# Optimization experiments

Measured on AMD Instinct MI355X. Metric: run time of the kernel, lower is better.

## Reference

```python
import jax, jax.numpy as jnp
import numpy as np

EPS = 1e-8  # args.epsilon
B, N, D = 2, 512, 64


def _cmul(ar, ai, br, bi):
    # complex Hadamard: (ar+i ai)(br+i bi)
    return ar * br - ai * bi, ar * bi + ai * br


def _clin(Z, W, b):
    # complex linear: Z [B,2,N,din], W [2,dout,din], b [2,dout]
    yr = Z[:, 0] @ W[0].T - Z[:, 1] @ W[1].T + b[0]
    yi = Z[:, 0] @ W[1].T + Z[:, 1] @ W[0].T + b[1]
    return yr, yi


def setup_inputs() -> dict:
    key = jax.random.key(0)
    ks = jax.random.split(key, 12)
    s = 1.0 / np.sqrt(D)
    inp = {
        "Z_q": jax.random.normal(ks[0], (B, 2, N, D), jnp.float32),
        "Z_k": jax.random.normal(ks[1], (B, 2, N, D), jnp.float32),
        "Z_v": jax.random.normal(ks[2], (B, 2, N, D), jnp.float32),
        "t_measure_all": (jnp.arange(N + 1, dtype=jnp.float32) / N)[None, :],
        "Wq_w": jax.random.normal(ks[3], (2, D, D), jnp.float32) * s,
        "Wq_b": jax.random.normal(ks[4], (2, D), jnp.float32) * 0.02,
        "Wk_w": jax.random.normal(ks[5], (2, D, D), jnp.float32) * s,
        "Wk_b": jax.random.normal(ks[6], (2, D), jnp.float32) * 0.02,
        "Wv_w": jax.random.normal(ks[7], (2, D, D), jnp.float32) * s,
        "Wv_b": jax.random.normal(ks[8], (2, D), jnp.float32) * 0.02,
        "Wp_w": jax.random.normal(ks[9], (2, D, D), jnp.float32) * s,
        "Wp_b": jax.random.normal(ks[10], (2, D), jnp.float32) * 0.02,
        "lambda_imag_v": jax.random.normal(ks[11], (D // 2,), jnp.float32),
        "lambda_omega_sqrt_v": jnp.asarray(0.5, jnp.float32),
        "lambda_gamma_sqrt_v": jnp.asarray(0.5, jnp.float32),
        "noise_floor": jnp.asarray(1.0, jnp.float32),
        "tau": jnp.asarray(1.0, jnp.float32),
        "eta_param": jnp.zeros((D,), jnp.float32),
    }
    return inp


def reference(Z_q, Z_k, Z_v, t_measure_all, Wq_w, Wq_b, Wk_w, Wk_b, Wv_w, Wv_b,
              Wp_w, Wp_b, lambda_imag_v, lambda_omega_sqrt_v, lambda_gamma_sqrt_v,
              noise_floor, tau, eta_param):
    n = Z_q.shape[2]
    # eigenvalues: lambda_real_zero==1 -> real part 0; conjugate imaginary pairs
    lam_imag = jnp.concatenate([lambda_imag_v, -lambda_imag_v])  # (D,)
    lambda_h = jnp.stack([jnp.zeros_like(lam_imag), lam_imag])   # (2, D)

    t = t_measure_all[0, :-1]
    t = t / (t[-1] - t[0])

    # exp kernels exp(+/- lambda t); real part 0 => pure phase
    ph = t[:, None] * lam_imag[None, :]            # (N, D)
    ef_r, ef_i = jnp.cos(ph), jnp.sin(ph)          # exp(+lambda t) (= V_v = V_k, mat_exp)
    eb_r, eb_i = ef_r, -ef_i                       # exp(-lambda t)

    Qr, Qi = _clin(Z_q, Wq_w, Wq_b)                # (B, N, D)
    Kr, Ki = _clin(Z_k, Wk_w, Wk_b)
    Vr, Vi = _clin(Z_v, Wv_w, Wv_b)

    # backward-propagated factors U = exp(-lambda t) o {Q,K,V}
    Uq_r, Uq_i = _cmul(eb_r, eb_i, Qr, Qi)
    Uk_r, Uk_i = _cmul(eb_r, eb_i, Kr, Ki)
    Uv_r, Uv_i = _cmul(eb_r, eb_i, Vr, Vi)

    # scalar covariance kernel (zero real part -> linear-in-|dt| variance)
    lambda_omega = lambda_omega_sqrt_v ** 2
    lambda_gamma = lambda_gamma_sqrt_v ** 2 + EPS
    V_avg = lambda_omega * jnp.abs(t[:, None] - t[None, :]) + lambda_gamma  # (N, N)

    # weighted residual norm R_ij = sum_d |V_k_i o (U_q_i - U_k_j)|^2, expanded
    W2 = ef_r ** 2 + ef_i ** 2                     # (N, D)  |V_k|^2
    aq2 = Uq_r ** 2 + Uq_i ** 2
    ak2 = Uk_r ** 2 + Uk_i ** 2
    t1 = jnp.einsum('id,bid->bi', W2, aq2)[:, :, None]
    t2 = jnp.einsum('id,bjd->bij', W2, ak2)
    t3 = (jnp.einsum('bid,bjd->bij', W2[None] * Uq_r, Uk_r)
          + jnp.einsum('bid,bjd->bij', W2[None] * Uq_i, Uk_i))
    R = t1 + t2 - 2.0 * t3                         # (B, N, N)

    base = (noise_floor ** 2 + EPS) * V_avg[None] + R
    scores = -(tau ** 2) * jnp.log(base)
    mask = jnp.tril(jnp.ones((n, n), bool))
    scores = jnp.where(mask[None], scores, -jnp.inf)
    A = jax.nn.softmax(scores, axis=2)             # (B, N, N)

    # est_inner = Q_ij @ U_v (Q_ij imag part is zero)
    er = jnp.einsum('bij,bjd->bid', A, Uv_r)
    ei = jnp.einsum('bij,bjd->bid', A, Uv_i)
    estv_r, estv_i = _cmul(ef_r, ef_i, er, ei)     # V_v o est_inner

    eta = jax.nn.sigmoid(eta_param)                # (D,)
    g = jax.nn.sigmoid(eta)                        # faithful double sigmoid
    elr = (1.0 - eta) * Vr + g * estv_r
    eli = (1.0 - eta) * Vi + g * estv_i

    pr, pi = _cmul(ef_r, ef_i, elr, eli)           # mat_exp o est_latent
    P = jnp.stack([pr, pi], axis=1)
    or_, oi_ = _clin(P, Wp_w, Wp_b)
    out = jnp.stack([or_, oi_], axis=1)            # (B, 2, N, D)

    est_latent = jnp.stack([elr, eli], axis=1)
    Q_ij = jnp.stack([A, jnp.zeros_like(A)], axis=1)
    # Z_ij_hat_all[b,:,i,j,d] = V_v_i o U_v_j  (propagated estimates)
    Zr = ef_r[None, :, None, :] * Uv_r[:, None] - ef_i[None, :, None, :] * Uv_i[:, None]
    Zi = ef_r[None, :, None, :] * Uv_i[:, None] + ef_i[None, :, None, :] * Uv_r[:, None]
    Z_ij_hat_all = jnp.stack([Zr, Zi], axis=1)     # (B, 2, N, N, D)

    return est_latent, out, Q_ij, Z_ij_hat_all, lambda_h
```

## Files before the change

kernel.cpp:

```cpp
#include <hip/hip_runtime.h>
#include <math.h>

#define NB 512
#define ND 64
#define EPSF 1e-8f

typedef float v4f __attribute__((ext_vector_type(4)));

__global__ __launch_bounds__(64) void proj_kernel(
    const float* __restrict__ Zq, const float* __restrict__ Zk, const float* __restrict__ Zv,
    const float* __restrict__ tma,
    const float* __restrict__ Wq_w, const float* __restrict__ Wq_b,
    const float* __restrict__ Wk_w, const float* __restrict__ Wk_b,
    const float* __restrict__ Wv_w, const float* __restrict__ Wv_b,
    const float* __restrict__ lam_v,
    float* __restrict__ ef_r, float* __restrict__ ef_i,
    float* __restrict__ Uq_r, float* __restrict__ Uq_i,
    float* __restrict__ Uk_r, float* __restrict__ Uk_i,
    float* __restrict__ Uv_r, float* __restrict__ Uv_i,
    float* __restrict__ Vr_o, float* __restrict__ Vi_o,
    float* __restrict__ sumq, float* __restrict__ sumk,
    float* __restrict__ lam_out)
{
    const int bn = blockIdx.x;
    const int b  = bn >> 9;
    const int n  = bn & (NB - 1);
    const int d  = threadIdx.x;

    __shared__ float zqr[ND], zqi[ND], zkr[ND], zki[ND], zvr[ND], zvi[ND];
    zqr[d] = Zq[((b*2 + 0)*NB + n)*ND + d];
    zqi[d] = Zq[((b*2 + 1)*NB + n)*ND + d];
    zkr[d] = Zk[((b*2 + 0)*NB + n)*ND + d];
    zki[d] = Zk[((b*2 + 1)*NB + n)*ND + d];
    zvr[d] = Zv[((b*2 + 0)*NB + n)*ND + d];
    zvi[d] = Zv[((b*2 + 1)*NB + n)*ND + d];
    __syncthreads();

    const float lam = (d < 32) ? lam_v[d] : -lam_v[d - 32];
    const float t0    = tma[0];
    const float denom = tma[NB - 1] - t0;
    const float tn    = tma[n] / denom;
    const float ph  = tn * lam;
    const float efr = cosf(ph);
    const float efi = sinf(ph);

    if (b == 0) { ef_r[n*ND + d] = efr; ef_i[n*ND + d] = efi; }
    if (bn == 0) { lam_out[d] = 0.0f; lam_out[ND + d] = lam; }

    float qr = Wq_b[d], qi = Wq_b[ND + d];
    float kr = Wk_b[d], ki = Wk_b[ND + d];
    float vr = Wv_b[d], vi = Wv_b[ND + d];
    const int r0 = d * ND;
    const int r1 = ND*ND + d * ND;
    #pragma unroll 8
    for (int e = 0; e < ND; ++e) {
        const float w0q = Wq_w[r0 + e], w1q = Wq_w[r1 + e];
        qr += zqr[e]*w0q - zqi[e]*w1q;
        qi += zqr[e]*w1q + zqi[e]*w0q;
        const float w0k = Wk_w[r0 + e], w1k = Wk_w[r1 + e];
        kr += zkr[e]*w0k - zki[e]*w1k;
        ki += zkr[e]*w1k + zki[e]*w0k;
        const float w0v = Wv_w[r0 + e], w1v = Wv_w[r1 + e];
        vr += zvr[e]*w0v - zvi[e]*w1v;
        vi += zvr[e]*w1v + zvi[e]*w0v;
    }

    const float uqr = efr*qr + efi*qi, uqi = efr*qi - efi*qr;
    const float ukr = efr*kr + efi*ki, uki = efr*ki - efi*kr;
    const float uvr = efr*vr + efi*vi, uvi = efr*vi - efi*vr;

    const int idx = bn*ND + d;
    Uq_r[idx] = uqr; Uq_i[idx] = uqi;
    Uk_r[idx] = ukr; Uk_i[idx] = uki;
    Uv_r[idx] = uvr; Uv_i[idx] = uvi;
    Vr_o[idx] = vr;  Vi_o[idx] = vi;

    float q2 = uqr*uqr + uqi*uqi;
    float k2 = ukr*ukr + uki*uki;
    #pragma unroll
    for (int off = 32; off > 0; off >>= 1) {
        q2 += __shfl_down(q2, off);
        k2 += __shfl_down(k2, off);
    }
    if (d == 0) { sumq[bn] = q2; sumk[bn] = k2; }
}

__global__ __launch_bounds__(256) void attn_fused_kernel(
    const float* __restrict__ ef_r, const float* __restrict__ ef_i,
    const float* __restrict__ Uq_r, const float* __restrict__ Uq_i,
    const float* __restrict__ Uk_r, const float* __restrict__ Uk_i,
    const float* __restrict__ Uv_r, const float* __restrict__ Uv_i,
    const float* __restrict__ Vr,  const float* __restrict__ Vi,
    const float* __restrict__ sumq, const float* __restrict__ sumk,
    const float* __restrict__ tma,
    const float* __restrict__ eta_param,
    const float* __restrict__ Wp_w, const float* __restrict__ Wp_b,
    const float* __restrict__ s_lo, const float* __restrict__ s_lg,
    const float* __restrict__ s_nf, const float* __restrict__ s_tau,
    float* __restrict__ estl_out,
    float* __restrict__ out_proj,
    float* __restrict__ Q_out,
    float* __restrict__ Z_out)
{
    const int bi  = blockIdx.x;
    const int b   = bi >> 9;
    const int i   = bi & (NB - 1);
    const int tid = threadIdx.x;

    __shared__ __align__(16) float sA[NB];
    __shared__ __align__(16) float qr_s[ND], qi_s[ND];
    __shared__ __align__(16) float efr_s[ND], efi_s[ND];
    __shared__ float red[256];
    __shared__ __align__(16) float erp[8][ND];
    __shared__ float pr_s[ND], pi_s[ND];

    const float t0    = tma[0];
    const float denom = tma[NB - 1] - t0;
    const float ti    = tma[i] / denom;
    const float lo    = s_lo[0] * s_lo[0];
    const float lg    = s_lg[0] * s_lg[0] + EPSF;
    const float nf2   = s_nf[0] * s_nf[0] + EPSF;
    const float tau2  = s_tau[0] * s_tau[0];
    const float t1    = sumq[bi];

    if (tid < ND) {
        qr_s[tid] = Uq_r[bi*ND + tid]; qi_s[tid] = Uq_i[bi*ND + tid];
    } else if (tid < 2*ND) {
        const int d = tid - ND;
        efr_s[d] = ef_r[i*ND + d]; efi_s[d] = ef_i[i*ND + d];
    }
    __syncthreads();

    float lmax = -INFINITY;
    for (int j = tid; j <= i; j += 256) {
        const float4* kr4 = (const float4*)&Uk_r[(b*NB + j)*ND];
        const float4* ki4 = (const float4*)&Uk_i[(b*NB + j)*ND];
        const float4* qr4 = (const float4*)qr_s;
        const float4* qi4 = (const float4*)qi_s;
        float dot = 0.0f;
        #pragma unroll
        for (int e = 0; e < ND/4; ++e) {
            const float4 kr = kr4[e], ki = ki4[e];
            const float4 qr = qr4[e], qi = qi4[e];
            dot += qr.x*kr.x + qr.y*kr.y + qr.z*kr.z + qr.w*kr.w
                 + qi.x*ki.x + qi.y*ki.y + qi.z*ki.z + qi.w*ki.w;
        }
        const float tj   = tma[j] / denom;
        const float vavg = lo * fabsf(ti - tj) + lg;
        const float base = nf2 * vavg + t1 + sumk[b*NB + j] - 2.0f*dot;
        const float sc   = -tau2 * logf(base);
        sA[j] = sc;
        lmax = fmaxf(lmax, sc);
    }

    red[tid] = lmax; __syncthreads();
    for (int s = 128; s > 0; s >>= 1) {
        if (tid < s) red[tid] = fmaxf(red[tid], red[tid + s]);
        __syncthreads();
    }
    const float m = red[0];
    __syncthreads();

    float lsum = 0.0f;
    for (int j = tid; j <= i; j += 256) {
        const float e = expf(sA[j] - m);
        sA[j] = e;
        lsum += e;
    }
    red[tid] = lsum; __syncthreads();
    for (int s = 128; s > 0; s >>= 1) {
        if (tid < s) red[tid] += red[tid + s];
        __syncthreads();
    }
    const float inv = 1.0f / red[0];
    __syncthreads();

    for (int j = tid; j < NB; j += 256) {
        float a = 0.0f;
        if (j <= i) { a = sA[j] * inv; sA[j] = a; }
        __builtin_nontemporal_store(a,    &Q_out[((size_t)(b*2 + 0)*NB + i)*NB + j]);
        __builtin_nontemporal_store(0.0f, &Q_out[((size_t)(b*2 + 1)*NB + i)*NB + j]);
    }
    __syncthreads();

    const int lane = tid & 63;
    const int w    = tid >> 6;
    float er = 0.0f, ei = 0.0f;
    for (int j = w; j <= i; j += 4) {
        const float a = sA[j];
        er += a * Uv_r[(b*NB + j)*ND + lane];
        ei += a * Uv_i[(b*NB + j)*ND + lane];
    }
    erp[w][lane] = er; erp[4 + w][lane] = ei;
    __syncthreads();

    if (tid < ND) {
        const int d = tid;
        const float err = erp[0][d] + erp[1][d] + erp[2][d] + erp[3][d];
        const float eii = erp[4][d] + erp[5][d] + erp[6][d] + erp[7][d];
        const float efr = efr_s[d], efi = efi_s[d];
        const float estr = efr*err - efi*eii;
        const float esti = efr*eii + efi*err;
        const float eta  = 1.0f / (1.0f + expf(-eta_param[d]));
        const float g    = 1.0f / (1.0f + expf(-eta));
        const float vr   = Vr[bi*ND + d], vi = Vi[bi*ND + d];
        const float elr  = (1.0f - eta)*vr + g*estr;
        const float eli  = (1.0f - eta)*vi + g*esti;
        estl_out[((b*2 + 0)*NB + i)*ND + d] = elr;
        estl_out[((b*2 + 1)*NB + i)*ND + d] = eli;
        pr_s[d] = efr*elr - efi*eli;
        pi_s[d] = efr*eli + efi*elr;
    }
    __syncthreads();

    {
        float po_r = 0.0f, po_i = 0.0f;
        const float* __restrict__ W0 = &Wp_w[lane*ND];
        const float* __restrict__ W1 = &Wp_w[ND*ND + lane*ND];
        const int e0 = w * (ND/4);
        #pragma unroll 4
        for (int e = e0; e < e0 + ND/4; ++e) {
            const float w0 = W0[e], w1 = W1[e];
            po_r += pr_s[e]*w0 - pi_s[e]*w1;
            po_i += pr_s[e]*w1 + pi_s[e]*w0;
        }
        erp[w][lane] = po_r; erp[4 + w][lane] = po_i;
    }
    __syncthreads();
    if (tid < ND) {
        const int d = tid;
        const float orr = Wp_b[d]      + erp[0][d] + erp[1][d] + erp[2][d] + erp[3][d];
        const float oii = Wp_b[ND + d] + erp[4][d] + erp[5][d] + erp[6][d] + erp[7][d];
        out_proj[((b*2 + 0)*NB + i)*ND + d] = orr;
        out_proj[((b*2 + 1)*NB + i)*ND + d] = oii;
    }

    const int d0    = (tid * 4) & (ND - 1);
    const int jbase = (tid * 4) >> 6;
    const float4 er4 = *(const float4*)&efr_s[d0];
    const float4 ei4 = *(const float4*)&efi_s[d0];

    const size_t base_r = ((size_t)(b*2 + 0)*NB + i) * (size_t)(NB*ND);
    const size_t base_i = ((size_t)(b*2 + 1)*NB + i) * (size_t)(NB*ND);
    const float* __restrict__ UvrB = &Uv_r[(size_t)(b*NB)*ND + d0];
    const float* __restrict__ UviB = &Uv_i[(size_t)(b*NB)*ND + d0];

    #pragma unroll 2
    for (int jg = 0; jg < NB; jg += 16) {
        const int j = jg + jbase;
        const float4 uvr = *(const float4*)&UvrB[(size_t)j*ND];
        const float4 uvi = *(const float4*)&UviB[(size_t)j*ND];
        v4f zr, zi;
        zr.x = er4.x*uvr.x - ei4.x*uvi.x;  zi.x = er4.x*uvi.x + ei4.x*uvr.x;
        zr.y = er4.y*uvr.y - ei4.y*uvi.y;  zi.y = er4.y*uvi.y + ei4.y*uvr.y;
        zr.z = er4.z*uvr.z - ei4.z*uvi.z;  zi.z = er4.z*uvi.z + ei4.z*uvr.z;
        zr.w = er4.w*uvr.w - ei4.w*uvi.w;  zi.w = er4.w*uvi.w + ei4.w*uvr.w;
        const size_t off = (size_t)j*ND + d0;
        __builtin_nontemporal_store(zr, (v4f*)&Z_out[base_r + off]);
        __builtin_nontemporal_store(zi, (v4f*)&Z_out[base_i + off]);
    }
}

extern "C" void kernel_launch(void* const* d_in, const int* in_sizes, int n_in,
                              void* d_out, int out_size, void* d_ws, size_t ws_size,
                              hipStream_t stream) {
    const float* Zq   = (const float*)d_in[0];
    const float* Zk   = (const float*)d_in[1];
    const float* Zv   = (const float*)d_in[2];
    const float* tma  = (const float*)d_in[3];
    const float* Wq_w = (const float*)d_in[4];
    const float* Wq_b = (const float*)d_in[5];
    const float* Wk_w = (const float*)d_in[6];
    const float* Wk_b = (const float*)d_in[7];
    const float* Wv_w = (const float*)d_in[8];
    const float* Wv_b = (const float*)d_in[9];
    const float* Wp_w = (const float*)d_in[10];
    const float* Wp_b = (const float*)d_in[11];
    const float* lamv = (const float*)d_in[12];
    const float* s_lo = (const float*)d_in[13];
    const float* s_lg = (const float*)d_in[14];
    const float* s_nf = (const float*)d_in[15];
    const float* s_tau= (const float*)d_in[16];
    const float* etap = (const float*)d_in[17];

    float* out = (float*)d_out;
    float* o_est = out;
    float* o_out = out + 131072;
    float* o_Q   = out + 262144;
    float* o_Z   = out + 1310720;
    float* o_lam = out + 68419584;

    float* ws   = (float*)d_ws;
    float* ef_r = ws;
    float* ef_i = ws + 32768;
    float* Uq_r = ws + 65536;
    float* Uq_i = ws + 131072;
    float* Uk_r = ws + 196608;
    float* Uk_i = ws + 262144;
    float* Uv_r = ws + 327680;
    float* Uv_i = ws + 393216;
    float* Vr   = ws + 458752;
    float* Vi   = ws + 524288;
    float* sumq = ws + 589824;
    float* sumk = ws + 590848;

    proj_kernel<<<2*NB, 64, 0, stream>>>(Zq, Zk, Zv, tma, Wq_w, Wq_b, Wk_w, Wk_b,
        Wv_w, Wv_b, lamv, ef_r, ef_i, Uq_r, Uq_i, Uk_r, Uk_i, Uv_r, Uv_i,
        Vr, Vi, sumq, sumk, o_lam);

    attn_fused_kernel<<<2*NB, 256, 0, stream>>>(ef_r, ef_i, Uq_r, Uq_i, Uk_r, Uk_i,
        Uv_r, Uv_i, Vr, Vi, sumq, sumk, tma, etap, Wp_w, Wp_b,
        s_lo, s_lg, s_nf, s_tau, o_est, o_out, o_Q, o_Z);
}
```

Before: 372.8 us.

## Fuse Z output write with A·Uv accumulation and use wave-shuffle reductions

The Z_ij_hat loop now also accumulates the attention-weighted Uv sums, so Uv is read once for both outputs instead of twice. sA is zero-filled beyond the causal limit to keep this correct. Block reductions for max and sum switch from shared-memory trees with many barriers to wave shuffles. Wp is staged into padded shared memory, a few scalar loads are hoisted before the first barrier, and the projection kernel reads its weights as float4. Staging Wp adds about 33KB of LDS per block, which may reduce occupancy.

Result: faster. 338.2 us (-9.3%).

```diff
diff --git a/kernel.cpp b/kernel.cpp
--- a/kernel.cpp
+++ b/kernel.cpp
@@ -52,17 +52,42 @@
     float vr = Wv_b[d], vi = Wv_b[ND + d];
     const int r0 = d * ND;
     const int r1 = ND*ND + d * ND;
-    #pragma unroll 8
-    for (int e = 0; e < ND; ++e) {
-        const float w0q = Wq_w[r0 + e], w1q = Wq_w[r1 + e];
-        qr += zqr[e]*w0q - zqi[e]*w1q;
-        qi += zqr[e]*w1q + zqi[e]*w0q;
-        const float w0k = Wk_w[r0 + e], w1k = Wk_w[r1 + e];
-        kr += zkr[e]*w0k - zki[e]*w1k;
-        ki += zkr[e]*w1k + zki[e]*w0k;
-        const float w0v = Wv_w[r0 + e], w1v = Wv_w[r1 + e];
-        vr += zvr[e]*w0v - zvi[e]*w1v;
-        vi += zvr[e]*w1v + zvi[e]*w0v;
+    const float4* __restrict__ wq0 = (const float4*)&Wq_w[r0];
+    const float4* __restrict__ wq1 = (const float4*)&Wq_w[r1];
+    const float4* __restrict__ wk0 = (const float4*)&Wk_w[r0];
+    const float4* __restrict__ wk1 = (const float4*)&Wk_w[r1];
+    const float4* __restrict__ wv0 = (const float4*)&Wv_w[r0];
+    const float4* __restrict__ wv1 = (const float4*)&Wv_w[r1];
+    #pragma unroll 4
+    for (int e4 = 0; e4 < ND/4; ++e4) {
+        const int e = e4 * 4;
+        const float4 q0 = wq0[e4], q1 = wq1[e4];
+        const float4 k0 = wk0[e4], k1 = wk1[e4];
+        const float4 v0 = wv0[e4], v1 = wv1[e4];
+        const float zr0 = zqr[e],   zi0 = zqi[e];
+        const float zr1 = zqr[e+1], zi1 = zqi[e+1];
+        const float zr2 = zqr[e+2], zi2 = zqi[e+2];
+        const float zr3 = zqr[e+3], zi3 = zqi[e+3];
+        qr += zr0*q0.x - zi0*q1.x;  qi += zr0*q1.x + zi0*q0.x;
+        qr += zr1*q0.y - zi1*q1.y;  qi += zr1*q1.y + zi1*q0.y;
+        qr += zr2*q0.z - zi2*q1.z;  qi += zr2*q1.z + zi2*q0.z;
+        qr += zr3*q0.w - zi3*q1.w;  qi += zr3*q1.w + zi3*q0.w;
+        const float yr0 = zkr[e],   yi0 = zki[e];
+        const float yr1 = zkr[e+1], yi1 = zki[e+1];
+        const float yr2 = zkr[e+2], yi2 = zki[e+2];
+        const float yr3 = zkr[e+3], yi3 = zki[e+3];
+        kr += yr0*k0.x - yi0*k1.x;  ki += yr0*k1.x + yi0*k0.x;
+        kr += yr1*k0.y - yi1*k1.y;  ki += yr1*k1.y + yi1*k0.y;
+        kr += yr2*k0.z - yi2*k1.z;  ki += yr2*k1.z + yi2*k0.z;
+        kr += yr3*k0.w - yi3*k1.w;  ki += yr3*k1.w + yi3*k0.w;
+        const float xr0 = zvr[e],   xi0 = zvi[e];
+        const float xr1 = zvr[e+1], xi1 = zvi[e+1];
+        const float xr2 = zvr[e+2], xi2 = zvi[e+2];
+        const float xr3 = zvr[e+3], xi3 = zvi[e+3];
+        vr += xr0*v0.x - xi0*v1.x;  vi += xr0*v1.x + xi0*v0.x;
+        vr += xr1*v0.y - xi1*v1.y;  vi += xr1*v1.y + xi1*v0.y;
+        vr += xr2*v0.z - xi2*v1.z;  vi += xr2*v1.z + xi2*v0.z;
+        vr += xr3*v0.w - xi3*v1.w;  vi += xr3*v1.w + xi3*v0.w;
     }
 
     const float uqr = efr*qr + efi*qi, uqi = efr*qi - efi*qr;
@@ -102,17 +127,22 @@
     float* __restrict__ Q_out,
     float* __restrict__ Z_out)
 {
-    const int bi  = blockIdx.x;
-    const int b   = bi >> 9;
-    const int i   = bi & (NB - 1);
-    const int tid = threadIdx.x;
+    const int bi   = blockIdx.x;
+    const int b    = bi >> 9;
+    const int i    = bi & (NB - 1);
+    const int tid  = threadIdx.x;
+    const int lane = tid & 63;
+    const int w    = tid >> 6;
+    const int sub  = lane >> 4;
+    const int d4   = (lane & 15) * 4;
 
     __shared__ __align__(16) float sA[NB];
     __shared__ __align__(16) float qr_s[ND], qi_s[ND];
     __shared__ __align__(16) float efr_s[ND], efi_s[ND];
-    __shared__ float red[256];
-    __shared__ __align__(16) float erp[8][ND];
-    __shared__ float pr_s[ND], pi_s[ND];
+    __shared__ float redmax[4], redsum[4];
+    __shared__ __align__(16) float erpr[4][ND], erpi[4][ND];
+    __shared__ __align__(16) float pr_s[ND], pi_s[ND];
+    __shared__ float wp_s[2][ND][ND + 1];
 
     const float t0    = tma[0];
     const float denom = tma[NB - 1] - t0;
@@ -128,6 +158,20 @@
     } else if (tid < 2*ND) {
         const int d = tid - ND;
         efr_s[d] = ef_r[i*ND + d]; efi_s[d] = ef_i[i*ND + d];
+    }
+    for (int idx = tid; idx < 2*ND*ND; idx += 256) {
+        const int pl = idx >> 12;
+        const int rr = (idx >> 6) & (ND - 1);
+        const int cc = idx & (ND - 1);
+        wp_s[pl][rr][cc] = Wp_w[idx];
+    }
+    float vr_reg = 0.f, vi_reg = 0.f, eta_raw = 0.f, wb0 = 0.f, wb1 = 0.f;
+    if (tid < ND) {
+        vr_reg  = Vr[bi*ND + tid];
+        vi_reg  = Vi[bi*ND + tid];
+        eta_raw = eta_param[tid];
+        wb0     = Wp_b[tid];
+        wb1     = Wp_b[ND + tid];
     }
     __syncthreads();
 
@@ -153,59 +197,87 @@
         lmax = fmaxf(lmax, sc);
     }
 
-    red[tid] = lmax; __syncthreads();
-    for (int s = 128; s > 0; s >>= 1) {
-        if (tid < s) red[tid] = fmaxf(red[tid], red[tid + s]);
-        __syncthreads();
-    }
-    const float m = red[0];
-    __syncthreads();
+    #pragma unroll
+    for (int m = 1; m < 64; m <<= 1) lmax = fmaxf(lmax, __shfl_xor(lmax, m));
+    if (lane == 0) redmax[w] = lmax;
+    __syncthreads();
+    const float mm = fmaxf(fmaxf(redmax[0], redmax[1]), fmaxf(redmax[2], redmax[3]));
 
     float lsum = 0.0f;
     for (int j = tid; j <= i; j += 256) {
-        const float e = expf(sA[j] - m);
+        const float e = expf(sA[j] - mm);
         sA[j] = e;
         lsum += e;
     }
-    red[tid] = lsum; __syncthreads();
-    for (int s = 128; s > 0; s >>= 1) {
-        if (tid < s) red[tid] += red[tid + s];
-        __syncthreads();
-    }
-    const float inv = 1.0f / red[0];
-    __syncthreads();
+    #pragma unroll
+    for (int m = 1; m < 64; m <<= 1) lsum += __shfl_xor(lsum, m);
+    if (lane == 0) redsum[w] = lsum;
+    __syncthreads();
+    const float inv = 1.0f / (redsum[0] + redsum[1] + redsum[2] + redsum[3]);
 
     for (int j = tid; j < NB; j += 256) {
         float a = 0.0f;
-        if (j <= i) { a = sA[j] * inv; sA[j] = a; }
+        if (j <= i) a = sA[j] * inv;
+        sA[j] = a;
         __builtin_nontemporal_store(a,    &Q_out[((size_t)(b*2 + 0)*NB + i)*NB + j]);
         __builtin_nontemporal_store(0.0f, &Q_out[((size_t)(b*2 + 1)*NB + i)*NB + j]);
     }
     __syncthreads();
 
-    const int lane = tid & 63;
-    const int w    = tid >> 6;
-    float er = 0.0f, ei = 0.0f;
-    for (int j = w; j <= i; j += 4) {
+    const float4 efr4 = *(const float4*)&efr_s[d4];
+    const float4 efi4 = *(const float4*)&efi_s[d4];
+    float erx = 0.f, ery = 0.f, erz = 0.f, erw = 0.f;
+    float eix = 0.f, eiy = 0.f, eiz = 0.f, eiw = 0.f;
+    const size_t base_r = ((size_t)(b*2 + 0)*NB + i) * (size_t)(NB*ND);
+    const size_t base_i = ((size_t)(b*2 + 1)*NB + i) * (size_t)(NB*ND);
+    const float* __restrict__ UvrB = &Uv_r[(size_t)(b*NB)*ND];
+    const float* __restrict__ UviB = &Uv_i[(size_t)(b*NB)*ND];
+    const int j0 = 4*w + sub;
+
+    #pragma unroll 4
+    for (int k = 0; k < NB/16; ++k) {
+        const int j = 16*k + j0;
+        const size_t roff = (size_t)j*ND + d4;
+        const float4 uvr = *(const float4*)&UvrB[roff];
+        const float4 uvi = *(const float4*)&UviB[roff];
+        v4f zr, zi;
+        zr.x = efr4.x*uvr.x - efi4.x*uvi.x;  zi.x = efr4.x*uvi.x + efi4.x*uvr.x;
+        zr.y = efr4.y*uvr.y - efi4.y*uvi.y;  zi.y = efr4.y*uvi.y + efi4.y*uvr.y;
+        zr.z = efr4.z*uvr.z - efi4.z*uvi.z;  zi.z = efr4.z*uvi.z + efi4.z*uvr.z;
+        zr.w = efr4.w*uvr.w - efi4.w*uvi.w;  zi.w = efr4.w*uvi.w + efi4.w*uvr.w;
+        __builtin_nontemporal_store(zr, (v4f*)&Z_out[base_r + roff]);
+        __builtin_nontemporal_store(zi, (v4f*)&Z_out[base_i + roff]);
         const float a = sA[j];
-        er += a * Uv_r[(b*NB + j)*ND + lane];
-        ei += a * Uv_i[(b*NB + j)*ND + lane];
-    }
-    erp[w][lane] = er; erp[4 + w][lane] = ei;
+        erx += a*uvr.x; ery += a*uvr.y; erz += a*uvr.z; erw += a*uvr.w;
+        eix += a*uvi.x; eiy += a*uvi.y; eiz += a*uvi.z; eiw += a*uvi.w;
+    }
+
+    #pragma unroll
+    for (int m = 16; m < 64; m <<= 1) {
+        erx += __shfl_xor(erx, m); ery += __shfl_xor(ery, m);
+        erz += __shfl_xor(erz, m); erw += __shfl_xor(erw, m);
+        eix += __shfl_xor(eix, m); eiy += __shfl_xor(eiy, m);
+        eiz += __shfl_xor(eiz, m); eiw += __shfl_xor(eiw, m);
+    }
+    if (lane < 16) {
+        float4 er4; er4.x = erx; er4.y = ery; er4.z = erz; er4.w = erw;
+        float4 ei4; ei4.x = eix; ei4.y = eiy; ei4.z = eiz; ei4.w = eiw;
+        *(float4*)&erpr[w][lane*4] = er4;
+        *(float4*)&erpi[w][lane*4] = ei4;
+    }
     __syncthreads();
 
     if (tid < ND) {
         const int d = tid;
-        const float err = erp[0][d] + erp[1][d] + erp[2][d] + erp[3][d];
-        const float eii = erp[4][d] + erp[5][d] + erp[6][d] + erp[7][d];
+        const float err = erpr[0][d] + erpr[1][d] + erpr[2][d] + erpr[3][d];
+        const float eii = erpi[0][d] + erpi[1][d] + erpi[2][d] + erpi[3][d];
         const float efr = efr_s[d], efi = efi_s[d];
         const float estr = efr*err - efi*eii;
         const float esti = efr*eii + efi*err;
-        const float eta  = 1.0f / (1.0f + expf(-eta_param[d]));
+        const float eta  = 1.0f / (1.0f + expf(-eta_raw));
         const float g    = 1.0f / (1.0f + expf(-eta));
-        const float vr   = Vr[bi*ND + d], vi = Vi[bi*ND + d];
-        const float elr  = (1.0f - eta)*vr + g*estr;
-        const float eli  = (1.0f - eta)*vi + g*esti;
+        const float elr  = (1.0f - eta)*vr_reg + g*estr;
+        const float eli  = (1.0f - eta)*vi_reg + g*esti;
         estl_out[((b*2 + 0)*NB + i)*ND + d] = elr;
         estl_out[((b*2 + 1)*NB + i)*ND + d] = eli;
         pr_s[d] = efr*elr - efi*eli;
@@ -215,49 +287,22 @@
 
     {
         float po_r = 0.0f, po_i = 0.0f;
-        const float* __restrict__ W0 = &Wp_w[lane*ND];
-        const float* __restrict__ W1 = &Wp_w[ND*ND + lane*ND];
         const int e0 = w * (ND/4);
         #pragma unroll 4
         for (int e = e0; e < e0 + ND/4; ++e) {
-            const float w0 = W0[e], w1 = W1[e];
+            const float w0 = wp_s[0][lane][e], w1 = wp_s[1][lane][e];
             po_r += pr_s[e]*w0 - pi_s[e]*w1;
             po_i += pr_s[e]*w1 + pi_s[e]*w0;
         }
-        erp[w][lane] = po_r; erp[4 + w][lane] = po_i;
+        erpr[w][lane] = po_r; erpi[w][lane] = po_i;
     }
     __syncthreads();
     if (tid < ND) {
         const int d = tid;
-        const float orr = Wp_b[d]      + erp[0][d] + erp[1][d] + erp[2][d] + erp[3][d];
-        const float oii = Wp_b[ND + d] + erp[4][d] + erp[5][d] + erp[6][d] + erp[7][d];
+        const float orr = wb0 + erpr[0][d] + erpr[1][d] + erpr[2][d] + erpr[3][d];
+        const float oii = wb1 + erpi[0][d] + erpi[1][d] + erpi[2][d] + erpi[3][d];
         out_proj[((b*2 + 0)*NB + i)*ND + d] = orr;
         out_proj[((b*2 + 1)*NB + i)*ND + d] = oii;
-    }
-
-    const int d0    = (tid * 4) & (ND - 1);
-    const int jbase = (tid * 4) >> 6;
-    const float4 er4 = *(const float4*)&efr_s[d0];
-    const float4 ei4 = *(const float4*)&efi_s[d0];
-
-    const size_t base_r = ((size_t)(b*2 + 0)*NB + i) * (size_t)(NB*ND);
-    const size_t base_i = ((size_t)(b*2 + 1)*NB + i) * (size_t)(NB*ND);
-    const float* __restrict__ UvrB = &Uv_r[(size_t)(b*NB)*ND + d0];
-    const float* __restrict__ UviB = &Uv_i[(size_t)(b*NB)*ND + d0];
-
-    #pragma unroll 2
-    for (int jg = 0; jg < NB; jg += 16) {
-        const int j = jg + jbase;
-        const float4 uvr = *(const float4*)&UvrB[(size_t)j*ND];
-        const float4 uvi = *(const float4*)&UviB[(size_t)j*ND];
-        v4f zr, zi;
-        zr.x = er4.x*uvr.x - ei4.x*uvi.x;  zi.x = er4.x*uvi.x + ei4.x*uvr.x;
-        zr.y = er4.y*uvr.y - ei4.y*uvi.y;  zi.y = er4.y*uvi.y + ei4.y*uvr.y;
-        zr.z = er4.z*uvr.z - ei4.z*uvi.z;  zi.z = er4.z*uvi.z + ei4.z*uvr.z;
-        zr.w = er4.w*uvr.w - ei4.w*uvi.w;  zi.w = er4.w*uvi.w + ei4.w*uvr.w;
-        const size_t off = (size_t)j*ND + d0;
-        __builtin_nontemporal_store(zr, (v4f*)&Z_out[base_r + off]);
-        __builtin_nontemporal_store(zi, (v4f*)&Z_out[base_i + off]);
     }
 }
 
```
